# Kernel tuning notes

Hardware: AMD Instinct MI355X
Metric: run time of the kernel (lower is better)

The kernel has to match this reference:

```python
import jax, jax.numpy as jnp
import numpy as np

G = 56          # voxel grid resolution per axis
N = 65536
K = 27          # 3x3x3 kernel offsets
C_IN = 128
C_OUT = 128


def _build_rulebook():
    """Submanifold conv rulebook: for each kernel offset, (input_row, output_row) pairs.

    Padded to P=N pairs per offset; invalid pairs use in_idx=0 and out_idx=N
    (a dummy output slot that is dropped), so shapes are static.
    """
    rng = np.random.default_rng(0)
    keys = np.sort(rng.choice(G ** 3, size=N, replace=False)).astype(np.int64)
    x = keys // (G * G)
    y = (keys // G) % G
    z = keys % G
    in_idx = np.zeros((K, N), dtype=np.int32)
    out_idx = np.full((K, N), N, dtype=np.int32)
    k = 0
    for dx in (-1, 0, 1):
        for dy in (-1, 0, 1):
            for dz in (-1, 0, 1):
                nx, ny, nz = x + dx, y + dy, z + dz
                valid = (nx >= 0) & (nx < G) & (ny >= 0) & (ny < G) & (nz >= 0) & (nz < G)
                nkey = (nx * G + ny) * G + nz
                pos = np.searchsorted(keys, np.clip(nkey, 0, G ** 3 - 1))
                pos = np.clip(pos, 0, N - 1)
                found = valid & (keys[pos] == nkey)
                cnt = int(found.sum())
                in_idx[k, :cnt] = pos[found]
                out_idx[k, :cnt] = np.nonzero(found)[0]
                k += 1
    return jnp.asarray(in_idx), jnp.asarray(out_idx)


def setup_inputs() -> dict:
    key = jax.random.key(0)
    k1, k2, k3 = jax.random.split(key, 3)
    fan_in = K * C_IN
    features = jax.random.normal(k1, (N, C_IN), dtype=jnp.float32)
    weight = jax.random.normal(k2, (K, C_IN, C_OUT), dtype=jnp.float32) * (1.0 / np.sqrt(fan_in))
    bias = jax.random.normal(k3, (C_OUT,), dtype=jnp.float32) * 0.01
    in_idx, out_idx = _build_rulebook()
    return {"features": features, "weight": weight, "bias": bias,
            "in_idx": in_idx, "out_idx": out_idx}


def reference(features, weight, bias, in_idx, out_idx):
    # gather: [K, P, C_in]
    gathered = features[in_idx]
    # per-offset GEMM: [K, P, C_out]
    contrib = jnp.einsum('kpc,kcd->kpd', gathered, weight)
    n = features.shape[0]
    c_out = weight.shape[-1]
    # scatter-accumulate into N real rows + 1 dummy row for padded pairs
    out = jnp.zeros((n + 1, c_out), dtype=features.dtype)
    out = out.at[out_idx.reshape(-1)].add(contrib.reshape(-1, c_out))
    return out[:n] + bias
```

## Files before the change

### kernel.cpp

```cpp
#include <hip/hip_runtime.h>
#include <hip/hip_bf16.h>
#include <stdint.h>

#define NV   65536
#define KOFF 27
#define CIN  128
#define COUT 128

typedef __bf16 bf16x8 __attribute__((ext_vector_type(8)));
typedef float  f32x4  __attribute__((ext_vector_type(4)));

__device__ __forceinline__ void async_copy16(void* lds, const void* g) {
    __builtin_amdgcn_global_load_lds(
        (const __attribute__((address_space(1))) void*)g,
        (__attribute__((address_space(3))) void*)lds,
        16, 0, 0);
}

#define JOB_A_BLOCKS 4097
#define JOB_B_BLOCKS 216
#define JOB_S_BLOCKS 1728

__global__ void k_prep_all(const float* __restrict__ f,
                           uint4* __restrict__ fb4,
                           const float* __restrict__ w,
                           uint4* __restrict__ wfrag4,
                           const int4* __restrict__ in4,
                           const int4* __restrict__ out4,
                           int* __restrict__ nbr) {
    const int b = blockIdx.x;
    const int t = threadIdx.x;
    if (b < JOB_A_BLOCKS) {
        int i = b * 256 + t;
        int total8  = (NV + 1) * CIN / 8;
        int nvalid8 = NV * CIN / 8;
        if (i >= total8) return;
        union { uint4 u; __hip_bfloat16 h[8]; } p;
        if (i < nvalid8) {
            const float4* f4 = (const float4*)f;
            float4 a = f4[i * 2];
            float4 c = f4[i * 2 + 1];
            p.h[0] = __float2bfloat16(a.x);
            p.h[1] = __float2bfloat16(a.y);
            p.h[2] = __float2bfloat16(a.z);
            p.h[3] = __float2bfloat16(a.w);
            p.h[4] = __float2bfloat16(c.x);
            p.h[5] = __float2bfloat16(c.y);
            p.h[6] = __float2bfloat16(c.z);
            p.h[7] = __float2bfloat16(c.w);
        } else {
            p.u = make_uint4(0, 0, 0, 0);
        }
        fb4[i] = p.u;
    } else if (b < JOB_A_BLOCKS + JOB_B_BLOCKS) {
        int c    = (b - JOB_A_BLOCKS) * 256 + t;
        int lane = c & 63;
        int nt   = (c >> 6) & 1;
        int ks   = (c >> 7) & 3;
        int wv   = (c >> 9) & 3;
        int k    = c >> 11;
        int cout = wv * 32 + nt * 16 + (lane & 15);
        int cin0 = ks * 32 + (lane >> 4) * 8;
        const float* wk = w + k * 16384;
        union { uint4 u; __hip_bfloat16 h[8]; } p;
        #pragma unroll
        for (int j = 0; j < 8; ++j)
            p.h[j] = __float2bfloat16(wk[(cin0 + j) * 128 + cout]);
        wfrag4[c] = p.u;
    } else {
        int i = (b - JOB_A_BLOCKS - JOB_B_BLOCKS) * 256 + t;
        int k = i >> 14;
        int4 ii = in4[i];
        int4 oo = out4[i];
        int* nb = nbr + k * (NV + 1);
        nb[oo.x] = ii.x;
        nb[oo.y] = ii.y;
        nb[oo.z] = ii.z;
        nb[oo.w] = ii.w;
    }
}

__global__ __launch_bounds__(256, 4)
void sp_conv_main(const __hip_bfloat16* __restrict__ feats,
                  const uint4* __restrict__ wfrag,
                  const int* __restrict__ nbr,
                  const float* __restrict__ bias,
                  float* __restrict__ out) {
    __shared__ unsigned char smem[32768];

    const int t   = threadIdx.x;
    const int bid = blockIdx.x;
    const int tile0 = ((bid & 7) * 128 + (bid >> 3)) * 64;

    const int w    = t >> 6;
    const int lane = t & 63;
    const int lr   = lane & 15;
    const int quad = lane >> 4;

    const int srow  = t >> 4;
    const int sbyte = ((t & 15) ^ srow) * 16;

    f32x4 acc[4][2] = {};

    const unsigned char* featsB = (const unsigned char*)feats;

    int  arows[4];
    uint4 bA[4][2], bB[4][2];

    auto AFLOAD = [&](int rb, int ks, bf16x8 (&af)[4]) {
        #pragma unroll
        for (int mt = 0; mt < 4; ++mt)
            af[mt] = *(const bf16x8*)(smem + rb + (mt * 16 + lr) * 256 +
                                      (((ks * 4 + quad) ^ lr) * 16));
    };
    auto MFMA8 = [&](bf16x8 (&af)[4], uint4 (&b)[2]) {
        #pragma unroll
        for (int mt = 0; mt < 4; ++mt)
            #pragma unroll
            for (int nt = 0; nt < 2; ++nt)
                acc[mt][nt] = __builtin_amdgcn_mfma_f32_16x16x32_bf16(
                    af[mt], *(const bf16x8*)&b[nt], acc[mt][nt], 0, 0, 0);
    };
    auto BLOAD = [&](const uint4* wfk, uint4 (&b)[4][2]) {
        #pragma unroll
        for (int ks = 0; ks < 4; ++ks)
            #pragma unroll
            for (int nt = 0; nt < 2; ++nt)
                b[ks][nt] = wfk[ks * 128 + nt * 64];
    };
    auto STAGE = [&](int sb) {
        #pragma unroll
        for (int i = 0; i < 4; ++i) {
            unsigned ar = min((unsigned)arows[i], (unsigned)NV);
            async_copy16(smem + sb + i * 4096 + t * 16,
                         featsB + (size_t)ar * 256 + sbyte);
        }
    };

    {
        const int* nbr0 = nbr + tile0;
        #pragma unroll
        for (int i = 0; i < 4; ++i) arows[i] = nbr0[i * 16 + srow];
    }
    STAGE(0);
    __builtin_amdgcn_sched_barrier(0);
    {
        const int* nbr1 = nbr + (NV + 1) + tile0;
        #pragma unroll
        for (int i = 0; i < 4; ++i) arows[i] = nbr1[i * 16 + srow];
    }
    BLOAD(wfrag + w * 512 + lane, bA);
    asm volatile("s_waitcnt vmcnt(12)" ::: "memory");
    __builtin_amdgcn_s_barrier();
    __builtin_amdgcn_sched_barrier(0);

    auto ITER = [&](int k, int rb, uint4 (&buse)[4][2], uint4 (&bload)[4][2]) {
        const int sb = rb ^ 16384;
        STAGE(sb);
        __builtin_amdgcn_sched_barrier(0);
        {
            const int* nbrn = nbr + min(k + 2, KOFF - 1) * (NV + 1) + tile0;
            #pragma unroll
            for (int i = 0; i < 4; ++i) arows[i] = nbrn[i * 16 + srow];
        }
        BLOAD(wfrag + (k + 1) * 2048 + w * 512 + lane, bload);
        #pragma unroll
        for (int ks = 0; ks < 4; ++ks) {
            bf16x8 af[4];
            AFLOAD(rb, ks, af);
            __builtin_amdgcn_s_setprio(1);
            MFMA8(af, buse[ks]);
            __builtin_amdgcn_s_setprio(0);
        }
        __builtin_amdgcn_sched_barrier(0);
        asm volatile("s_waitcnt vmcnt(12)" ::: "memory");
        __builtin_amdgcn_s_barrier();
        __builtin_amdgcn_sched_barrier(0);
    };

    #pragma unroll 1
    for (int kk = 0; kk < KOFF - 1; kk += 2) {
        ITER(kk,     0,     bA, bB);
        ITER(kk + 1, 16384, bB, bA);
    }

    #pragma unroll
    for (int ks = 0; ks < 4; ++ks) {
        bf16x8 af[4];
        AFLOAD(0, ks, af);
        MFMA8(af, bA[ks]);
    }

    const int n0w = w * 32;
    float bv[2];
    #pragma unroll
    for (int nt = 0; nt < 2; ++nt) bv[nt] = bias[n0w + nt * 16 + lr];

    #pragma unroll
    for (int mt = 0; mt < 4; ++mt) {
        #pragma unroll
        for (int nt = 0; nt < 2; ++nt) {
            #pragma unroll
            for (int r = 0; r < 4; ++r) {
                int grow = tile0 + mt * 16 + quad * 4 + r;
                out[(size_t)grow * COUT + n0w + nt * 16 + lr] =
                    acc[mt][nt][r] + bv[nt];
            }
        }
    }
}


extern "C" void kernel_launch(void* const* d_in, const int* in_sizes, int n_in,
                              void* d_out, int out_size, void* d_ws, size_t ws_size,
                              hipStream_t stream) {
    const float* features = (const float*)d_in[0];
    const float* weight   = (const float*)d_in[1];
    const float* bias     = (const float*)d_in[2];
    const int*   in_idx   = (const int*)d_in[3];
    const int*   out_idx  = (const int*)d_in[4];
    float* out = (float*)d_out;

    uint8_t* ws = (uint8_t*)d_ws;
    size_t off = 0;
    __hip_bfloat16* feats_bf = (__hip_bfloat16*)(ws + off);
    off += (size_t)(NV + 1) * CIN * 2;
    off = (off + 255) & ~(size_t)255;
    uint4* wfrag = (uint4*)(ws + off);
    off += (size_t)KOFF * CIN * COUT * 2;
    off = (off + 255) & ~(size_t)255;
    int* nbr = (int*)(ws + off);

    hipMemsetAsync(nbr, 0xFF, (size_t)KOFF * (NV + 1) * 4, stream);

    k_prep_all<<<JOB_A_BLOCKS + JOB_B_BLOCKS + JOB_S_BLOCKS, 256, 0, stream>>>(
        features, (uint4*)feats_bf, weight, wfrag,
        (const int4*)in_idx, (const int4*)out_idx, nbr);

    sp_conv_main<<<NV / 64, 256, 0, stream>>>(feats_bf, wfrag, nbr, bias, out);
}
```

Before: 176.3 us.

## Double output tile to 128 rows per block with permuted neighbor table layout

Each block now computes 128 output rows instead of 64, which halves how often each weight fragment is loaded from global memory per output row and doubles the MFMA work per barrier. The neighbor table is written in a permuted layout so each thread fetches its 8 gather row indices with two int4 loads instead of scalar loads. LDS per block doubles to 64KB and occupancy drops to 2 blocks per CU. The grid shrinks to 512 blocks, which may leave the 256 CUs underfilled and reduce latency hiding.

```diff
diff --git a/kernel.cpp b/kernel.cpp
--- a/kernel.cpp
+++ b/kernel.cpp
@@ -6,6 +6,7 @@
 #define KOFF 27
 #define CIN  128
 #define COUT 128
+#define NSEC (NV + 128)
 
 typedef __bf16 bf16x8 __attribute__((ext_vector_type(8)));
 typedef float  f32x4  __attribute__((ext_vector_type(4)));
@@ -72,25 +73,28 @@
         int k = i >> 14;
         int4 ii = in4[i];
         int4 oo = out4[i];
-        int* nb = nbr + k * (NV + 1);
-        nb[oo.x] = ii.x;
-        nb[oo.y] = ii.y;
-        nb[oo.z] = ii.z;
-        nb[oo.w] = ii.w;
-    }
-}
-
-__global__ __launch_bounds__(256, 4)
+        int* nb = nbr + (size_t)k * NSEC;
+        auto POS = [](int o) {
+            return (o >> 7) * 128 + (o & 15) * 8 + ((o >> 4) & 7);
+        };
+        nb[POS(oo.x)] = ii.x;
+        nb[POS(oo.y)] = ii.y;
+        nb[POS(oo.z)] = ii.z;
+        nb[POS(oo.w)] = ii.w;
+    }
+}
+
+__global__ __launch_bounds__(256, 2)
 void sp_conv_main(const __hip_bfloat16* __restrict__ feats,
                   const uint4* __restrict__ wfrag,
-                  const int* __restrict__ nbr,
+                  const int* __restrict__ nbrt,
                   const float* __restrict__ bias,
                   float* __restrict__ out) {
-    __shared__ unsigned char smem[32768];
+    __shared__ unsigned char smem[65536];
 
     const int t   = threadIdx.x;
     const int bid = blockIdx.x;
-    const int tile0 = ((bid & 7) * 128 + (bid >> 3)) * 64;
+    const int tile0 = ((bid & 7) * 64 + (bid >> 3)) * 128;
 
     const int w    = t >> 6;
     const int lane = t & 63;
@@ -100,80 +104,74 @@
     const int srow  = t >> 4;
     const int sbyte = ((t & 15) ^ srow) * 16;
 
-    f32x4 acc[4][2] = {};
+    f32x4 acc[8][2] = {};
 
     const unsigned char* featsB = (const unsigned char*)feats;
 
-    int  arows[4];
+    int  arows[8];
     uint4 bA[4][2], bB[4][2];
 
-    auto AFLOAD = [&](int rb, int ks, bf16x8 (&af)[4]) {
-        #pragma unroll
-        for (int mt = 0; mt < 4; ++mt)
+    auto NLOAD = [&](int k) {
+        const int4* np = (const int4*)(nbrt + (size_t)k * NSEC + tile0 + srow * 8);
+        int4 a0 = np[0];
+        int4 a1 = np[1];
+        arows[0] = a0.x; arows[1] = a0.y; arows[2] = a0.z; arows[3] = a0.w;
+        arows[4] = a1.x; arows[5] = a1.y; arows[6] = a1.z; arows[7] = a1.w;
+    };
+    auto STAGE = [&](int sb) {
+        #pragma unroll
+        for (int i = 0; i < 8; ++i) {
+            unsigned ar = min((unsigned)arows[i], (unsigned)NV);
+            async_copy16(smem + sb + i * 4096 + t * 16,
+                         featsB + (size_t)ar * 256 + sbyte);
+        }
+    };
+    auto BLOAD = [&](const uint4* wfk, uint4 (&b)[4][2]) {
+        #pragma unroll
+        for (int ks = 0; ks < 4; ++ks)
+            #pragma unroll
+            for (int nt = 0; nt < 2; ++nt)
+                b[ks][nt] = wfk[ks * 128 + nt * 64];
+    };
+    auto AFLOAD = [&](int rb, int ks, bf16x8 (&af)[8]) {
+        #pragma unroll
+        for (int mt = 0; mt < 8; ++mt)
             af[mt] = *(const bf16x8*)(smem + rb + (mt * 16 + lr) * 256 +
                                       (((ks * 4 + quad) ^ lr) * 16));
     };
-    auto MFMA8 = [&](bf16x8 (&af)[4], uint4 (&b)[2]) {
-        #pragma unroll
-        for (int mt = 0; mt < 4; ++mt)
+    auto MFMA16 = [&](bf16x8 (&af)[8], uint4 (&b)[2]) {
+        #pragma unroll
+        for (int mt = 0; mt < 8; ++mt)
             #pragma unroll
             for (int nt = 0; nt < 2; ++nt)
                 acc[mt][nt] = __builtin_amdgcn_mfma_f32_16x16x32_bf16(
                     af[mt], *(const bf16x8*)&b[nt], acc[mt][nt], 0, 0, 0);
     };
-    auto BLOAD = [&](const uint4* wfk, uint4 (&b)[4][2]) {
-        #pragma unroll
-        for (int ks = 0; ks < 4; ++ks)
-            #pragma unroll
-            for (int nt = 0; nt < 2; ++nt)
-                b[ks][nt] = wfk[ks * 128 + nt * 64];
-    };
-    auto STAGE = [&](int sb) {
-        #pragma unroll
-        for (int i = 0; i < 4; ++i) {
-            unsigned ar = min((unsigned)arows[i], (unsigned)NV);
-            async_copy16(smem + sb + i * 4096 + t * 16,
-                         featsB + (size_t)ar * 256 + sbyte);
-        }
-    };
-
-    {
-        const int* nbr0 = nbr + tile0;
-        #pragma unroll
-        for (int i = 0; i < 4; ++i) arows[i] = nbr0[i * 16 + srow];
-    }
+
+    NLOAD(0);
     STAGE(0);
     __builtin_amdgcn_sched_barrier(0);
-    {
-        const int* nbr1 = nbr + (NV + 1) + tile0;
-        #pragma unroll
-        for (int i = 0; i < 4; ++i) arows[i] = nbr1[i * 16 + srow];
-    }
+    NLOAD(1);
     BLOAD(wfrag + w * 512 + lane, bA);
-    asm volatile("s_waitcnt vmcnt(12)" ::: "memory");
+    asm volatile("s_waitcnt vmcnt(10)" ::: "memory");
     __builtin_amdgcn_s_barrier();
     __builtin_amdgcn_sched_barrier(0);
 
     auto ITER = [&](int k, int rb, uint4 (&buse)[4][2], uint4 (&bload)[4][2]) {
-        const int sb = rb ^ 16384;
-        STAGE(sb);
+        STAGE(rb ^ 32768);
         __builtin_amdgcn_sched_barrier(0);
-        {
-            const int* nbrn = nbr + min(k + 2, KOFF - 1) * (NV + 1) + tile0;
-            #pragma unroll
-            for (int i = 0; i < 4; ++i) arows[i] = nbrn[i * 16 + srow];
-        }
+        NLOAD(min(k + 2, KOFF - 1));
         BLOAD(wfrag + (k + 1) * 2048 + w * 512 + lane, bload);
         #pragma unroll
         for (int ks = 0; ks < 4; ++ks) {
-            bf16x8 af[4];
+            bf16x8 af[8];
             AFLOAD(rb, ks, af);
             __builtin_amdgcn_s_setprio(1);
-            MFMA8(af, buse[ks]);
+            MFMA16(af, buse[ks]);
             __builtin_amdgcn_s_setprio(0);
         }
         __builtin_amdgcn_sched_barrier(0);
-        asm volatile("s_waitcnt vmcnt(12)" ::: "memory");
+        asm volatile("s_waitcnt vmcnt(10)" ::: "memory");
         __builtin_amdgcn_s_barrier();
         __builtin_amdgcn_sched_barrier(0);
     };
@@ -181,14 +179,14 @@
     #pragma unroll 1
     for (int kk = 0; kk < KOFF - 1; kk += 2) {
         ITER(kk,     0,     bA, bB);
-        ITER(kk + 1, 16384, bB, bA);
+        ITER(kk + 1, 32768, bB, bA);
     }
 
     #pragma unroll
     for (int ks = 0; ks < 4; ++ks) {
-        bf16x8 af[4];
+        bf16x8 af[8];
         AFLOAD(0, ks, af);
-        MFMA8(af, bA[ks]);
+        MFMA16(af, bA[ks]);
     }
 
     const int n0w = w * 32;
@@ -197,7 +195,7 @@
     for (int nt = 0; nt < 2; ++nt) bv[nt] = bias[n0w + nt * 16 + lr];
 
     #pragma unroll
-    for (int mt = 0; mt < 4; ++mt) {
+    for (int mt = 0; mt < 8; ++mt) {
         #pragma unroll
         for (int nt = 0; nt < 2; ++nt) {
             #pragma unroll
@@ -231,11 +229,11 @@
     off = (off + 255) & ~(size_t)255;
     int* nbr = (int*)(ws + off);
 
-    hipMemsetAsync(nbr, 0xFF, (size_t)KOFF * (NV + 1) * 4, stream);
+    hipMemsetAsync(nbr, 0xFF, (size_t)KOFF * NSEC * 4, stream);
 
     k_prep_all<<<JOB_A_BLOCKS + JOB_B_BLOCKS + JOB_S_BLOCKS, 256, 0, stream>>>(
         features, (uint4*)feats_bf, weight, wfrag,
         (const int4*)in_idx, (const int4*)out_idx, nbr);
 
-    sp_conv_main<<<NV / 64, 256, 0, stream>>>(feats_bf, wfrag, nbr, bias, out);
-}
+    sp_conv_main<<<NV / 128, 256, 0, stream>>>(feats_bf, wfrag, nbr, bias, out);
+}
```

New measurement: 151.6 us. -14.0%, faster.
